# Optimization experiments

Hardware: AMD Instinct MI355X
Metric: run time of the kernel (lower is better)

Reference implementation:

```python
import jax, jax.numpy as jnp
import numpy as np

B, N, G, K, C, H, L = 16, 8192, 128, 32, 384, 6, 12
HID = 4 * C
EPS = 1e-5

def _pairwise_sq(a, b):
    # squared euclidean distances (B, M, N); same argsort order as torch.cdist
    d = (jnp.sum(a * a, -1)[:, :, None] + jnp.sum(b * b, -1)[:, None, :]
         - 2.0 * jnp.einsum('bmd,bnd->bmn', a, b))
    return jnp.maximum(d, 0.0)

def _fps(xyz, npoint):
    # deterministic farthest point sampling (start index 0), per torch loop
    bsz, n = xyz.shape[0], xyz.shape[1]
    def step(carry, _):
        distance, farthest = carry
        centroid = jnp.take_along_axis(xyz, farthest[:, None, None], axis=1)  # (B,1,3)
        d = jnp.sum((xyz - centroid) ** 2, axis=-1)
        distance = jnp.minimum(distance, d)
        nxt = jnp.argmax(distance, axis=-1).astype(jnp.int32)
        return (distance, nxt), farthest
    init = (jnp.full((bsz, n), 1e10, jnp.float32), jnp.zeros((bsz,), jnp.int32))
    _, cents = jax.lax.scan(step, init, None, length=npoint)
    return cents.T  # (B, npoint)

def _nearest_order(center):
    # greedy nearest-neighbor path over patch centers starting at 0
    bsz, g = center.shape[0], center.shape[1]
    d2 = _pairwise_sq(center, center)
    diag = jnp.arange(g)
    d2 = d2.at[:, diag, diag].set(jnp.inf)
    bi = jnp.arange(bsz)
    visited0 = jnp.zeros((bsz, g), bool).at[:, 0].set(True)
    def step(carry, _):
        last, visited = carry
        d = jnp.where(visited, jnp.inf, d2[bi, last])
        nxt = jnp.argmin(d, axis=-1).astype(jnp.int32)
        return (nxt, visited.at[bi, nxt].set(True)), nxt
    _, rest = jax.lax.scan(step, (jnp.zeros((bsz,), jnp.int32), visited0), None, length=g - 1)
    return jnp.concatenate([jnp.zeros((bsz, 1), jnp.int32), rest.T], axis=1)

def _bn(x, g, b):
    # BatchNorm1d, training-mode batch statistics over (batch, length)
    m = x.mean(axis=(0, 1))
    v = x.var(axis=(0, 1))
    return (x - m) * jax.lax.rsqrt(v + EPS) * g + b

def _ln(x, g, b):
    m = x.mean(-1, keepdims=True)
    v = x.var(-1, keepdims=True)
    return (x - m) * jax.lax.rsqrt(v + EPS) * g + b

def _pos_sine(coords, d_model):
    # sine/cosine positional embedding per coordinate channel (DETR-style)
    d_per = d_model // coords.shape[-1]  # 128 per xyz channel
    inv = 1.0 / (10000.0 ** (2.0 * jnp.arange(d_per // 2, dtype=jnp.float32) / d_per))
    ang = coords[..., None] * inv  # (B,G,3,d_per//2)
    emb = jnp.stack([jnp.sin(ang), jnp.cos(ang)], axis=-1)
    return emb.reshape(coords.shape[0], coords.shape[1], d_model)

def _block(x, mask, ln1g, ln1b, qkvw, qkvb, ow, ob, ln2g, ln2b, m1w, m1b, m2w, m2b):
    bsz, s, c = x.shape
    dh = c // H
    y = _ln(x, ln1g, ln1b)
    qkv = y @ qkvw.T + qkvb
    q, k, v = [t.reshape(bsz, s, H, dh) for t in jnp.split(qkv, 3, axis=-1)]
    scores = jnp.einsum('bqhd,bkhd->bhqk', q, k) / np.sqrt(dh)
    scores = jnp.where(mask, scores, -1e9)  # causal attn_mask
    attn = jax.nn.softmax(scores, axis=-1)
    o = jnp.einsum('bhqk,bkhd->bqhd', attn, v).reshape(bsz, s, c)
    x = x + o @ ow.T + ob
    h = jax.nn.gelu(_ln(x, ln2g, ln2b) @ m1w.T + m1b, approximate=False)
    return x + h @ m2w.T + m2b

def _forward(xyz, ec1_w, ec1_b, bn1_g, bn1_b, ec2_w, ec2_b, sc1_w, sc1_b,
             bn2_g, bn2_b, sc2_w, sc2_b, sos, ln1_g, ln1_b, qkv_w, qkv_b,
             out_w, out_b, ln2_g, ln2_b, mlp1_w, mlp1_b, mlp2_w, mlp2_b,
             lnf_g, lnf_b):
    bsz = xyz.shape[0]
    # --- Group: FPS centers + kNN neighborhoods + nearest-path ordering ---
    cent_idx = _fps(xyz, G)                                         # (B,G)
    center = jnp.take_along_axis(xyz, cent_idx[..., None], axis=1)  # (B,G,3)
    d2 = _pairwise_sq(center, xyz)                                  # (B,G,N)
    _, knn = jax.lax.top_k(-d2, K)                                  # smallest distances
    neigh = jnp.take_along_axis(xyz, knn.reshape(bsz, G * K)[..., None], axis=1)
    neigh = neigh.reshape(bsz, G, K, 3) - center[:, :, None, :]
    order = _nearest_order(center)
    neigh = jnp.take_along_axis(neigh, order[:, :, None, None], axis=1)
    center = jnp.take_along_axis(center, order[:, :, None], axis=1)
    # --- EncoderSmall (1x1 convs == pointwise matmuls + max pooling) ---
    x = neigh.reshape(bsz * G, K, 3)
    f = jax.nn.relu(_bn(x @ ec1_w.T + ec1_b, bn1_g, bn1_b))
    f = f @ ec2_w.T + ec2_b                                         # (BG,K,256)
    gmax = f.max(axis=1, keepdims=True)
    f = jnp.concatenate([jnp.broadcast_to(gmax, f.shape), f], axis=-1)  # (BG,K,512)
    f = jax.nn.relu(_bn(f @ sc1_w.T + sc1_b, bn2_g, bn2_b))
    f = f @ sc2_w.T + sc2_b
    tokens = f.max(axis=1).reshape(bsz, G, C)
    # --- GPT extractor: sos-shifted tokens, pos added per layer, causal ---
    pos = _pos_sine(center, C)
    mask = jnp.tril(jnp.ones((G, G), bool))
    h = jnp.concatenate([jnp.broadcast_to(sos, (bsz, 1, C)), tokens[:, :-1]], axis=1)
    for i in range(L):
        h = _block(h + pos, mask, ln1_g[i], ln1_b[i], qkv_w[i], qkv_b[i],
                   out_w[i], out_b[i], ln2_g[i], ln2_b[i], mlp1_w[i], mlp1_b[i],
                   mlp2_w[i], mlp2_b[i])
    return _ln(h, lnf_g, lnf_b)

def setup_inputs():
    key = jax.random.key(0)
    ks = jax.random.split(key, 12)
    w = lambda k, shape: jax.random.normal(k, shape, jnp.float32) * 0.02
    return {
        'xyz': jax.random.normal(ks[0], (B, N, 3), jnp.float32),
        'ec1_w': w(ks[1], (128, 3)), 'ec1_b': jnp.zeros((128,)),
        'bn1_g': jnp.ones((128,)), 'bn1_b': jnp.zeros((128,)),
        'ec2_w': w(ks[2], (256, 128)), 'ec2_b': jnp.zeros((256,)),
        'sc1_w': w(ks[3], (512, 512)), 'sc1_b': jnp.zeros((512,)),
        'bn2_g': jnp.ones((512,)), 'bn2_b': jnp.zeros((512,)),
        'sc2_w': w(ks[4], (C, 512)), 'sc2_b': jnp.zeros((C,)),
        'sos': w(ks[5], (1, 1, C)),
        'ln1_g': jnp.ones((L, C)), 'ln1_b': jnp.zeros((L, C)),
        'qkv_w': w(ks[6], (L, 3 * C, C)), 'qkv_b': jnp.zeros((L, 3 * C)),
        'out_w': w(ks[7], (L, C, C)), 'out_b': jnp.zeros((L, C)),
        'ln2_g': jnp.ones((L, C)), 'ln2_b': jnp.zeros((L, C)),
        'mlp1_w': w(ks[8], (L, HID, C)), 'mlp1_b': jnp.zeros((L, HID)),
        'mlp2_w': w(ks[9], (L, C, HID)), 'mlp2_b': jnp.zeros((L, C)),
        'lnf_g': jnp.ones((C,)), 'lnf_b': jnp.zeros((C,)),
    }

def reference(xyz, ec1_w, ec1_b, bn1_g, bn1_b, ec2_w, ec2_b, sc1_w, sc1_b,
              bn2_g, bn2_b, sc2_w, sc2_b, sos, ln1_g, ln1_b, qkv_w, qkv_b,
              out_w, out_b, ln2_g, ln2_b, mlp1_w, mlp1_b, mlp2_w, mlp2_b,
              lnf_g, lnf_b):
    return _forward(xyz, ec1_w, ec1_b, bn1_g, bn1_b, ec2_w, ec2_b, sc1_w, sc1_b,
                    bn2_g, bn2_b, sc2_w, sc2_b, sos, ln1_g, ln1_b, qkv_w, qkv_b,
                    out_w, out_b, ln2_g, ln2_b, mlp1_w, mlp1_b, mlp2_w, mlp2_b,
                    lnf_g, lnf_b)
```

## Files before the change

### kernel.cpp

```cpp
#include <hip/hip_runtime.h>
#include <math.h>

#define DEVFN __device__ __forceinline__

constexpr int NB   = 16;
constexpr int NPTS = 8192;
constexpr int NG   = 128;
constexpr int NK   = 32;
constexpr int NC   = 384;
constexpr int NH   = 6;
constexpr int NL   = 12;
constexpr int NHID = 1536;
constexpr int NDH  = 64;
constexpr float LN_EPS = 1e-5f;

typedef __attribute__((ext_vector_type(8))) short short8v;
typedef __attribute__((ext_vector_type(4))) float f32x4;
typedef unsigned long long u64;

DEVFN float sq3(float x, float y, float z) {
  return __fadd_rn(__fadd_rn(__fmul_rn(x, x), __fmul_rn(y, y)), __fmul_rn(z, z));
}
DEVFN float dot3(float ax, float ay, float az, float bx, float by, float bz) {
  return __fadd_rn(__fadd_rn(__fmul_rn(ax, bx), __fmul_rn(ay, by)), __fmul_rn(az, bz));
}
DEVFN unsigned short f2bf(float f) {
  unsigned u = __float_as_uint(f);
  return (unsigned short)((u + 0x7fffu + ((u >> 16) & 1u)) >> 16);
}
DEVFN float bf2f(unsigned short u) { return __uint_as_float(((unsigned)u) << 16); }

__global__ __launch_bounds__(512) void fps_kernel(const float* __restrict__ xyz,
                                                  int* __restrict__ cent) {
  extern __shared__ float dsm[];
  float* lx = dsm; float* ly = dsm + NPTS; float* lz = dsm + 2 * NPTS;
  __shared__ u64 swk[2][8];
  const int b = blockIdx.x, t = threadIdx.x;
  const float* X = xyz + (size_t)b * NPTS * 3;
  float px[16], py[16], pz[16], dd[16];
#pragma unroll
  for (int k = 0; k < 16; ++k) {
    const int i = t + k * 512;
    px[k] = X[i * 3 + 0]; py[k] = X[i * 3 + 1]; pz[k] = X[i * 3 + 2];
    lx[i] = px[k]; ly[i] = py[k]; lz[i] = pz[k];
    dd[k] = 1e10f;
  }
  __syncthreads();
  int far = 0;
  float fx = lx[0], fy = ly[0], fz = lz[0];
  for (int s = 0; s < NG; ++s) {
    if (t == 0) cent[b * NG + s] = far;
    float bv = -1.0f; int bi = 0;
#pragma unroll
    for (int k = 0; k < 16; ++k) {
      const float dx = __fsub_rn(px[k], fx);
      const float dy = __fsub_rn(py[k], fy);
      const float dz = __fsub_rn(pz[k], fz);
      const float d  = sq3(dx, dy, dz);
      const float nd = fminf(dd[k], d);
      dd[k] = nd;
      if (nd > bv) { bv = nd; bi = t + k * 512; }
    }
    u64 key = (((u64)__float_as_uint(bv)) << 32) | (unsigned)(8191 - bi);
#pragma unroll
    for (int m = 1; m < 64; m <<= 1) {
      const u64 o = __shfl_xor(key, m, 64);
      key = (o > key) ? o : key;
    }
    if ((t & 63) == 0) swk[s & 1][t >> 6] = key;
    __syncthreads();
    u64 fk = swk[s & 1][0];
#pragma unroll
    for (int w = 1; w < 8; ++w) fk = (swk[s & 1][w] > fk) ? swk[s & 1][w] : fk;
    far = 8191 - (int)(fk & 0xffffffffu);
    fx = lx[far]; fy = ly[far]; fz = lz[far];
  }
}

__global__ __launch_bounds__(256) void knn_kernel(const float* __restrict__ xyz,
                                                  const int* __restrict__ cent,
                                                  float* __restrict__ center,
                                                  int* __restrict__ knn) {
  __shared__ u64 swk[2][4];
  __shared__ float sc[3];
  const int bg = blockIdx.x, t = threadIdx.x;
  const int b = bg >> 7;
  const float* X = xyz + (size_t)b * NPTS * 3;
  if (t == 0) {
    const int ci = cent[bg];
    sc[0] = X[ci * 3 + 0]; sc[1] = X[ci * 3 + 1]; sc[2] = X[ci * 3 + 2];
    center[bg * 3 + 0] = sc[0]; center[bg * 3 + 1] = sc[1]; center[bg * 3 + 2] = sc[2];
  }
  __syncthreads();
  const float cx = sc[0], cy = sc[1], cz = sc[2];
  const float ra = sq3(cx, cy, cz);
  float d[32];
#pragma unroll
  for (int k = 0; k < 32; ++k) {
    const int i = t + k * 256;
    const float x = X[i * 3 + 0], y = X[i * 3 + 1], z = X[i * 3 + 2];
    const float rb = sq3(x, y, z);
    const float dt = dot3(cx, cy, cz, x, y, z);
    d[k] = fmaxf(__fsub_rn(__fadd_rn(ra, rb), __fmul_rn(2.0f, dt)), 0.0f);
  }
  float lv = 3.0e38f; int li = 0;
#pragma unroll
  for (int k = 0; k < 32; ++k) { if (d[k] < lv) { lv = d[k]; li = k; } }
  for (int k = 0; k < NK; ++k) {
    u64 key = (((u64)__float_as_uint(lv)) << 32) | (unsigned)(t + li * 256);
#pragma unroll
    for (int m = 1; m < 64; m <<= 1) {
      const u64 o = __shfl_xor(key, m, 64);
      key = (o < key) ? o : key;
    }
    if ((t & 63) == 0) swk[k & 1][t >> 6] = key;
    __syncthreads();
    u64 fk = swk[k & 1][0];
#pragma unroll
    for (int w = 1; w < 4; ++w) fk = (swk[k & 1][w] < fk) ? swk[k & 1][w] : fk;
    const int fi = (int)(fk & 0xffffffffu);
    if (t == 0) knn[(size_t)bg * NK + k] = fi;
    if ((fi & 255) == t) {
      const int kk = fi >> 8;
#pragma unroll
      for (int j = 0; j < 32; ++j) if (j == kk) d[j] = 3.0e38f;
      lv = 3.0e38f; li = 0;
#pragma unroll
      for (int j = 0; j < 32; ++j) { if (d[j] < lv) { lv = d[j]; li = j; } }
    }
  }
}

__global__ __launch_bounds__(128) void order_kernel(const float* __restrict__ center,
                                                    int* __restrict__ order) {
  __shared__ float cx[NG], cy[NG], cz[NG];
  __shared__ u64 swk[2][2];
  const int b = blockIdx.x, t = threadIdx.x;
  cx[t] = center[((size_t)b * NG + t) * 3 + 0];
  cy[t] = center[((size_t)b * NG + t) * 3 + 1];
  cz[t] = center[((size_t)b * NG + t) * 3 + 2];
  bool vis = (t == 0);
  if (t == 0) order[b * NG] = 0;
  __syncthreads();
  int last = 0;
  for (int s = 1; s < NG; ++s) {
    float dv;
    const float lx = cx[last], ly = cy[last], lz = cz[last];
    if (vis) {
      dv = 3.0e38f;
    } else {
      const float ra = sq3(lx, ly, lz), rb = sq3(cx[t], cy[t], cz[t]);
      const float dd = __fsub_rn(__fadd_rn(ra, rb),
                                 __fmul_rn(2.0f, dot3(lx, ly, lz, cx[t], cy[t], cz[t])));
      dv = fmaxf(dd, 0.0f);
    }
    u64 key = (((u64)__float_as_uint(dv)) << 32) | (unsigned)t;
#pragma unroll
    for (int m = 1; m < 64; m <<= 1) {
      const u64 o = __shfl_xor(key, m, 64);
      key = (o < key) ? o : key;
    }
    if ((t & 63) == 0) swk[s & 1][t >> 6] = key;
    __syncthreads();
    const u64 fk = (swk[s & 1][1] < swk[s & 1][0]) ? swk[s & 1][1] : swk[s & 1][0];
    last = (int)(fk & 0xffffffffu);
    if (t == last) vis = true;
    if (t == 0) order[b * NG + s] = last;
  }
}

__global__ void gather_neigh(const float* __restrict__ xyz, const int* __restrict__ knn,
                             const int* __restrict__ order, const float* __restrict__ center,
                             float* __restrict__ neigh, float* __restrict__ cord) {
  const int bg = blockIdx.x, t = threadIdx.x;
  const int b = bg >> 7;
  const int src = order[bg];
  const int sbg = (b << 7) + src;
  const float c0 = center[sbg * 3 + 0], c1 = center[sbg * 3 + 1], c2 = center[sbg * 3 + 2];
  if (t < 3) cord[bg * 3 + t] = center[sbg * 3 + t];
  const int idx = knn[(size_t)sbg * NK + t];
  const float* P = xyz + ((size_t)b * NPTS + idx) * 3;
  float* o = neigh + ((size_t)bg * NK + t) * 3;
  o[0] = __fsub_rn(P[0], c0);
  o[1] = __fsub_rn(P[1], c1);
  o[2] = __fsub_rn(P[2], c2);
}

__global__ __launch_bounds__(128) void bn1_stats(const float* __restrict__ neigh,
                                                 const float* __restrict__ w,
                                                 const float* __restrict__ bias,
                                                 float* __restrict__ psum,
                                                 float* __restrict__ psq) {
  const int c = threadIdx.x, blk = blockIdx.x;
  const float wx = w[c * 3 + 0], wy = w[c * 3 + 1], wz = w[c * 3 + 2], bb = bias[c];
  float s = 0.f, s2 = 0.f;
  const float* nr = neigh + (size_t)blk * 256 * 3;
  for (int r = 0; r < 256; ++r) {
    float y = fmaf(nr[r * 3 + 2], wz, fmaf(nr[r * 3 + 1], wy, fmaf(nr[r * 3 + 0], wx, bb)));
    s += y; s2 = fmaf(y, y, s2);
  }
  psum[c * 256 + blk] = s;
  psq[c * 256 + blk]  = s2;
}

__global__ __launch_bounds__(256) void bn_reduce(const float* __restrict__ psum,
                                                 const float* __restrict__ psq,
                                                 const float* __restrict__ g,
                                                 const float* __restrict__ b,
                                                 float* __restrict__ A, float* __restrict__ B0,
                                                 int P) {
  __shared__ double rs[256], rq[256];
  const int c = blockIdx.x, t = threadIdx.x;
  double s = 0.0, q = 0.0;
  for (int i = t; i < P; i += 256) {
    s += (double)psum[(size_t)c * P + i];
    q += (double)psq[(size_t)c * P + i];
  }
  rs[t] = s; rq[t] = q;
  __syncthreads();
  for (int o = 128; o > 0; o >>= 1) {
    if (t < o) { rs[t] += rs[t + o]; rq[t] += rq[t + o]; }
    __syncthreads();
  }
  if (t == 0) {
    const double M = 65536.0;
    double m = rs[0] / M;
    double v = rq[0] / M - m * m;
    if (v < 0) v = 0;
    float a = g[c] * rsqrtf((float)v + LN_EPS);
    A[c] = a;
    B0[c] = b[c] - (float)m * a;
  }
}

__global__ __launch_bounds__(256) void enc_f1(const float* __restrict__ neigh,
                                              const float* __restrict__ ec1w, const float* __restrict__ ec1b,
                                              const float* __restrict__ A1, const float* __restrict__ B01,
                                              unsigned short* __restrict__ f1bf) {
  __shared__ float ns[96];
  const int bg = blockIdx.x, t = threadIdx.x;
  if (t < 96) ns[t] = neigh[(size_t)bg * 96 + t];
  __syncthreads();
  for (int e = t; e < 32 * 128; e += 256) {
    const int r = e >> 7, c = e & 127;
    float y = fmaf(ns[r * 3 + 2], ec1w[c * 3 + 2],
             fmaf(ns[r * 3 + 1], ec1w[c * 3 + 1],
             fmaf(ns[r * 3 + 0], ec1w[c * 3 + 0], ec1b[c])));
    y = fmaxf(fmaf(y, A1[c], B01[c]), 0.f);
    f1bf[(size_t)bg * 4096 + e] = f2bf(y);
  }
}

template <int K, int NTILE, int EPI>
__global__ __launch_bounds__(256) void enc_gemm(const unsigned short* __restrict__ A,
                                                const unsigned short* __restrict__ W,
                                                const float* __restrict__ bias,
                                                const float* __restrict__ sgbuf,
                                                const float* __restrict__ A2,
                                                const float* __restrict__ B02,
                                                unsigned short* __restrict__ C,
                                                unsigned short* __restrict__ gmaxOut,
                                                float* __restrict__ psum,
                                                float* __restrict__ psq,
                                                const float* __restrict__ sc2b,
                                                float* __restrict__ tokens) {
  constexpr int LDA = K + 8;
  __shared__ unsigned short At[64 * LDA];
  const int blk = blockIdx.x, t = threadIdx.x;
  const int m0 = blk * 64;
  for (int idx = t; idx < 64 * (K / 8); idx += 256) {
    const int row = idx / (K / 8), off = idx % (K / 8);
    short8v v = *(const short8v*)(A + (size_t)(m0 + row) * K + off * 8);
    if (EPI == 2) {
      float a2v[8], b0v[8];
      *(float4*)(a2v)     = *(const float4*)(A2 + off * 8);
      *(float4*)(a2v + 4) = *(const float4*)(A2 + off * 8 + 4);
      *(float4*)(b0v)     = *(const float4*)(B02 + off * 8);
      *(float4*)(b0v + 4) = *(const float4*)(B02 + off * 8 + 4);
#pragma unroll
      for (int j = 0; j < 8; ++j)
        v[j] = (short)f2bf(fmaxf(fmaf(bf2f((unsigned short)v[j]), a2v[j], b0v[j]), 0.f));
    }
    *(short8v*)(At + row * LDA + off * 8) = v;
  }
  __syncthreads();
  const int lane = t & 63, wid = t >> 6;
  const int wr = wid >> 1, wc = wid & 1;
  const int lr = lane & 15, kg = lane >> 4;
  const int group = 2 * blk + wr;
  const unsigned short* a0 = At + (wr * 32 + lr) * LDA + kg * 8;
  const unsigned short* a1 = a0 + 16 * LDA;
  for (int nt = 0; nt < NTILE / 64; ++nt) {
    const int n0 = nt * 64 + wc * 32;
    const unsigned short* b0 = W + (size_t)(n0 + lr) * K + kg * 8;
    const unsigned short* b1 = b0 + (size_t)16 * K;
    f32x4 acc00 = {0.f, 0.f, 0.f, 0.f}, acc01 = acc00, acc10 = acc00, acc11 = acc00;
#pragma unroll
    for (int k0 = 0; k0 < K; k0 += 32) {
      const short8v av0 = *(const short8v*)(a0 + k0);
      const short8v av1 = *(const short8v*)(a1 + k0);
      const short8v bv0 = *(const short8v*)(b0 + k0);
      const short8v bv1 = *(const short8v*)(b1 + k0);
      acc00 = __builtin_amdgcn_mfma_f32_16x16x32_bf16(av0, bv0, acc00, 0, 0, 0);
      acc01 = __builtin_amdgcn_mfma_f32_16x16x32_bf16(av0, bv1, acc01, 0, 0, 0);
      acc10 = __builtin_amdgcn_mfma_f32_16x16x32_bf16(av1, bv0, acc10, 0, 0, 0);
      acc11 = __builtin_amdgcn_mfma_f32_16x16x32_bf16(av1, bv1, acc11, 0, 0, 0);
    }
#pragma unroll
    for (int j = 0; j < 2; ++j) {
      const int n = n0 + j * 16 + lr;
      float red0 = (EPI == 1) ? 0.f : -3.0e38f;
      float red1 = 0.f;
      float base = 0.f;
      if (EPI == 0) base = bias[n];
      if (EPI == 1) base = bias[n] + sgbuf[(size_t)group * NTILE + n];
#pragma unroll
      for (int i = 0; i < 2; ++i) {
        const f32x4 a = (i == 0) ? (j == 0 ? acc00 : acc01) : (j == 0 ? acc10 : acc11);
#pragma unroll
        for (int r = 0; r < 4; ++r) {
          const int m = m0 + wr * 32 + i * 16 + kg * 4 + r;
          const float v = a[r] + base;
          if (EPI == 0) {
            C[(size_t)m * NTILE + n] = f2bf(v);
            red0 = fmaxf(red0, v);
          } else if (EPI == 1) {
            const unsigned short us = f2bf(v);
            C[(size_t)m * NTILE + n] = us;
            const float vv = bf2f(us);
            red0 += vv; red1 = fmaf(vv, vv, red1);
          } else {
            red0 = fmaxf(red0, v);
          }
        }
      }
      if (EPI == 1) {
        red0 += __shfl_xor(red0, 16, 64); red0 += __shfl_xor(red0, 32, 64);
        red1 += __shfl_xor(red1, 16, 64); red1 += __shfl_xor(red1, 32, 64);
        if (kg == 0) {
          psum[(size_t)n * 2048 + blk * 2 + wr] = red0;
          psq[(size_t)n * 2048 + blk * 2 + wr]  = red1;
        }
      } else {
        red0 = fmaxf(red0, __shfl_xor(red0, 16, 64));
        red0 = fmaxf(red0, __shfl_xor(red0, 32, 64));
        if (kg == 0) {
          if (EPI == 0) gmaxOut[(size_t)group * NTILE + n] = f2bf(red0);
          else          tokens[(size_t)group * NTILE + n] = red0 + sc2b[n];
        }
      }
    }
  }
}

__global__ void pos_hinit(const float* __restrict__ cord, const float* __restrict__ tokens,
                          const float* __restrict__ sos,
                          float* __restrict__ pos, float* __restrict__ h) {
  const int tok = blockIdx.x, t = threadIdx.x;
  const int c = t >> 7;
  const int rem = t & 127;
  const int i = rem >> 1;
  const int isc = rem & 1;
  const float coord = cord[tok * 3 + c];
  const float ex = 2.0f * (float)i / 128.0f;
  const float inv = 1.0f / powf(10000.0f, ex);
  const float ang = coord * inv;
  pos[(size_t)tok * NC + t] = isc ? cosf(ang) : sinf(ang);
  const int b = tok >> 7, g = tok & 127;
  h[(size_t)tok * NC + t] = (g == 0) ? sos[t] : tokens[((size_t)b * NG + (g - 1)) * NC + t];
}

__global__ void cvt_all(const float* __restrict__ qkvw, const float* __restrict__ outw,
                        const float* __restrict__ m1w, const float* __restrict__ m2w,
                        const float* __restrict__ ec2w, const float* __restrict__ sc1w,
                        const float* __restrict__ sc2w,
                        unsigned short* __restrict__ wqkv, unsigned short* __restrict__ wout,
                        unsigned short* __restrict__ wm1, unsigned short* __restrict__ wm2,
                        unsigned short* __restrict__ ec2, unsigned short* __restrict__ w3a,
                        unsigned short* __restrict__ w3b, unsigned short* __restrict__ sc2) {
  constexpr int S0 = NL * 3 * NC * NC;
  constexpr int O0 = S0;
  constexpr int O1 = O0 + NL * NC * NC;
  constexpr int O2 = O1 + NL * NHID * NC;
  constexpr int O3 = O2 + NL * NC * NHID;
  constexpr int O4 = O3 + 256 * 128;
  constexpr int O5 = O4 + 512 * 512;
  constexpr int TOT = O5 + 384 * 512;
  for (int i = blockIdx.x * blockDim.x + threadIdx.x; i < TOT; i += gridDim.x * blockDim.x) {
    if (i < O0)      wqkv[i] = f2bf(qkvw[i]);
    else if (i < O1) wout[i - O0] = f2bf(outw[i - O0]);
    else if (i < O2) wm1[i - O1] = f2bf(m1w[i - O1]);
    else if (i < O3) wm2[i - O2] = f2bf(m2w[i - O2]);
    else if (i < O4) ec2[i - O3] = f2bf(ec2w[i - O3]);
    else if (i < O5) {
      const int ii = i - O4, c = ii >> 9, k = ii & 511;
      const unsigned short v = f2bf(sc1w[ii]);
      if (k < 256) w3a[c * 256 + k] = v;
      else         w3b[c * 256 + (k - 256)] = v;
    } else sc2[i - O5] = f2bf(sc2w[i - O5]);
  }
}

template <bool BF16OUT>
__global__ __launch_bounds__(128) void ln_kernel(const float* __restrict__ in,
                                                 const float* __restrict__ add,
                                                 const float* __restrict__ g,
                                                 const float* __restrict__ b,
                                                 void* __restrict__ y,
                                                 float* __restrict__ xout) {
  __shared__ float sm[4];
  const int row = blockIdx.x, t = threadIdx.x, w = t >> 6;
  const float* ip = in + (size_t)row * NC;
  float v0 = ip[t], v1 = ip[t + 128], v2 = ip[t + 256];
  if (add) {
    const float* ap = add + (size_t)row * NC;
    v0 += ap[t]; v1 += ap[t + 128]; v2 += ap[t + 256];
  }
  float s = v0 + v1 + v2;
#pragma unroll
  for (int m = 1; m < 64; m <<= 1) s += __shfl_xor(s, m, 64);
  if ((t & 63) == 0) sm[w] = s;
  __syncthreads();
  const float mean = (sm[0] + sm[1]) / (float)NC;
  const float d0 = v0 - mean, d1 = v1 - mean, d2 = v2 - mean;
  float sq = d0 * d0 + d1 * d1 + d2 * d2;
#pragma unroll
  for (int m = 1; m < 64; m <<= 1) sq += __shfl_xor(sq, m, 64);
  if ((t & 63) == 0) sm[2 + w] = sq;
  __syncthreads();
  const float rs = rsqrtf((sm[2] + sm[3]) / (float)NC + LN_EPS);
  const float y0 = d0 * rs * g[t] + b[t];
  const float y1 = d1 * rs * g[t + 128] + b[t + 128];
  const float y2 = d2 * rs * g[t + 256] + b[t + 256];
  if (BF16OUT) {
    unsigned short* yp = (unsigned short*)y + (size_t)row * NC;
    yp[t] = f2bf(y0); yp[t + 128] = f2bf(y1); yp[t + 256] = f2bf(y2);
  } else {
    float* yp = (float*)y + (size_t)row * NC;
    yp[t] = y0; yp[t + 128] = y1; yp[t + 256] = y2;
  }
  if (xout) {
    float* xp = xout + (size_t)row * NC;
    xp[t] = v0; xp[t + 128] = v1; xp[t + 256] = v2;
  }
}

template <int ACT, int RESMODE, bool OUT_BF, int K>
__global__ __launch_bounds__(256) void gemm_mfma(const unsigned short* __restrict__ A,
                                                 const unsigned short* __restrict__ W,
                                                 const float* __restrict__ bias,
                                                 const float* __restrict__ R,
                                                 void* __restrict__ Cv,
                                                 int N) {
  const int t = threadIdx.x;
  const int lane = t & 63, wid = t >> 6;
  const int wr = wid >> 1, wc = wid & 1;
  const int m0 = blockIdx.y * 64 + wr * 32;
  const int n0 = blockIdx.x * 64 + wc * 32;
  const int lr = lane & 15, kg = lane >> 4;
  const unsigned short* a0p = A + (size_t)(m0 + lr) * K + kg * 8;
  const unsigned short* a1p = a0p + (size_t)16 * K;
  const unsigned short* b0p = W + (size_t)(n0 + lr) * K + kg * 8;
  const unsigned short* b1p = b0p + (size_t)16 * K;
  f32x4 acc00 = {0.f, 0.f, 0.f, 0.f}, acc01 = acc00, acc10 = acc00, acc11 = acc00;
#pragma unroll 2
  for (int k0 = 0; k0 < K; k0 += 32) {
    const short8v av0 = *(const short8v*)(a0p + k0);
    const short8v av1 = *(const short8v*)(a1p + k0);
    const short8v bv0 = *(const short8v*)(b0p + k0);
    const short8v bv1 = *(const short8v*)(b1p + k0);
    acc00 = __builtin_amdgcn_mfma_f32_16x16x32_bf16(av0, bv0, acc00, 0, 0, 0);
    acc01 = __builtin_amdgcn_mfma_f32_16x16x32_bf16(av0, bv1, acc01, 0, 0, 0);
    acc10 = __builtin_amdgcn_mfma_f32_16x16x32_bf16(av1, bv0, acc10, 0, 0, 0);
    acc11 = __builtin_amdgcn_mfma_f32_16x16x32_bf16(av1, bv1, acc11, 0, 0, 0);
  }
#pragma unroll
  for (int i = 0; i < 2; ++i) {
#pragma unroll
    for (int j = 0; j < 2; ++j) {
      const f32x4 a = (i == 0) ? (j == 0 ? acc00 : acc01) : (j == 0 ? acc10 : acc11);
      const int n = n0 + j * 16 + lr;
      const float bn = bias ? bias[n] : 0.f;
#pragma unroll
      for (int r = 0; r < 4; ++r) {
        const int m = m0 + i * 16 + kg * 4 + r;
        float v = a[r] + bn;
        if (ACT == 1) v = 0.5f * v * (1.0f + erff(v * 0.70710678118654752f));
        if (RESMODE == 1) v += R[(size_t)m * N + n];
        if (OUT_BF) ((unsigned short*)Cv)[(size_t)m * N + n] = f2bf(v);
        else        ((float*)Cv)[(size_t)m * N + n] = v;
      }
    }
  }
}

__global__ __launch_bounds__(256) void attn_fused(const unsigned short* __restrict__ qkv,
                                                  unsigned short* __restrict__ obuf) {
  __shared__ __align__(16) unsigned short qs[64 * 72];
  __shared__ __align__(16) unsigned short ks[128 * 72];
  __shared__ __align__(16) unsigned short vt[64 * 136];
  __shared__ __align__(16) unsigned short ps[64 * 136];
  const int blk = blockIdx.x, t = threadIdx.x;
  const int qt = blk & 1;
  const int h = (blk >> 1) % NH;
  const int b = blk / (2 * NH);
  const size_t qbase = ((size_t)(b * NG + qt * 64)) * (3 * NC) + h * NDH;
  const size_t kbase = ((size_t)(b * NG)) * (3 * NC) + NC + h * NDH;
  const size_t vbase = kbase + NC;
#pragma unroll
  for (int it = 0; it < 2; ++it) {
    const int idx = t + it * 256;
    const int r = idx >> 3, c0 = (idx & 7) * 8;
    *(short8v*)(qs + r * 72 + c0) = *(const short8v*)(qkv + qbase + (size_t)r * (3 * NC) + c0);
  }
#pragma unroll
  for (int it = 0; it < 4; ++it) {
    const int idx = t + it * 256;
    const int r = idx >> 3, c0 = (idx & 7) * 8;
    *(short8v*)(ks + r * 72 + c0) = *(const short8v*)(qkv + kbase + (size_t)r * (3 * NC) + c0);
  }
#pragma unroll
  for (int it = 0; it < 4; ++it) {
    const int idx = t + it * 256;
    const int r = idx >> 3, c0 = (idx & 7) * 8;
    const short8v v = *(const short8v*)(qkv + vbase + (size_t)r * (3 * NC) + c0);
#pragma unroll
    for (int j = 0; j < 8; ++j) vt[(c0 + j) * 136 + r] = (unsigned short)v[j];
  }
  __syncthreads();
  const int lane = t & 63, w = t >> 6;
  const int lr = lane & 15, kg = lane >> 4;
  f32x4 sc[8] = {};
  {
    const short8v av0 = *(const short8v*)(qs + (w * 16 + lr) * 72 + kg * 8);
    const short8v av1 = *(const short8v*)(qs + (w * 16 + lr) * 72 + 32 + kg * 8);
#pragma unroll
    for (int j = 0; j < 8; ++j) {
      const short8v bv0 = *(const short8v*)(ks + (j * 16 + lr) * 72 + kg * 8);
      const short8v bv1 = *(const short8v*)(ks + (j * 16 + lr) * 72 + 32 + kg * 8);
      sc[j] = __builtin_amdgcn_mfma_f32_16x16x32_bf16(av0, bv0, sc[j], 0, 0, 0);
      sc[j] = __builtin_amdgcn_mfma_f32_16x16x32_bf16(av1, bv1, sc[j], 0, 0, 0);
    }
  }
#pragma unroll
  for (int r = 0; r < 4; ++r) {
    const int rowg = qt * 64 + w * 16 + kg * 4 + r;
    float pj[8];
    float mx = -3.0e38f;
#pragma unroll
    for (int j = 0; j < 8; ++j) {
      const int col = j * 16 + lr;
      const float s = (col <= rowg) ? sc[j][r] * 0.125f : -1e9f;
      pj[j] = s;
      mx = fmaxf(mx, s);
    }
#pragma unroll
    for (int m = 1; m < 16; m <<= 1) mx = fmaxf(mx, __shfl_xor(mx, m, 64));
    float sum = 0.f;
#pragma unroll
    for (int j = 0; j < 8; ++j) { pj[j] = expf(pj[j] - mx); sum += pj[j]; }
#pragma unroll
    for (int m = 1; m < 16; m <<= 1) sum += __shfl_xor(sum, m, 64);
#pragma unroll
    for (int j = 0; j < 8; ++j)
      ps[(w * 16 + kg * 4 + r) * 136 + j * 16 + lr] = f2bf(pj[j] / sum);
  }
  __syncthreads();
  f32x4 oc[4] = {};
#pragma unroll
  for (int k = 0; k < 4; ++k) {
    const short8v av = *(const short8v*)(ps + (w * 16 + lr) * 136 + k * 32 + kg * 8);
#pragma unroll
    for (int dj = 0; dj < 4; ++dj) {
      const short8v bv = *(const short8v*)(vt + (dj * 16 + lr) * 136 + k * 32 + kg * 8);
      oc[dj] = __builtin_amdgcn_mfma_f32_16x16x32_bf16(av, bv, oc[dj], 0, 0, 0);
    }
  }
#pragma unroll
  for (int dj = 0; dj < 4; ++dj) {
#pragma unroll
    for (int r = 0; r < 4; ++r) {
      const int m = qt * 64 + w * 16 + kg * 4 + r;
      obuf[((size_t)(b * NG + m)) * NC + h * NDH + dj * 16 + lr] = f2bf(oc[dj][r]);
    }
  }
}

extern "C" void kernel_launch(void* const* d_in, const int* in_sizes, int n_in,
                              void* d_out, int out_size, void* d_ws, size_t ws_size,
                              hipStream_t stream) {
  (void)in_sizes; (void)n_in; (void)out_size; (void)ws_size;
  const float* xyz  = (const float*)d_in[0];
  const float* ec1w = (const float*)d_in[1];
  const float* ec1b = (const float*)d_in[2];
  const float* bn1g = (const float*)d_in[3];
  const float* bn1b = (const float*)d_in[4];
  const float* ec2w = (const float*)d_in[5];
  const float* ec2b = (const float*)d_in[6];
  const float* sc1w = (const float*)d_in[7];
  const float* sc1b = (const float*)d_in[8];
  const float* bn2g = (const float*)d_in[9];
  const float* bn2b = (const float*)d_in[10];
  const float* sc2w = (const float*)d_in[11];
  const float* sc2b = (const float*)d_in[12];
  const float* sos  = (const float*)d_in[13];
  const float* ln1g = (const float*)d_in[14];
  const float* ln1b = (const float*)d_in[15];
  const float* qkvw = (const float*)d_in[16];
  const float* qkvb = (const float*)d_in[17];
  const float* outw = (const float*)d_in[18];
  const float* outb = (const float*)d_in[19];
  const float* ln2g = (const float*)d_in[20];
  const float* ln2b = (const float*)d_in[21];
  const float* m1w  = (const float*)d_in[22];
  const float* m1b  = (const float*)d_in[23];
  const float* m2w  = (const float*)d_in[24];
  const float* m2b  = (const float*)d_in[25];
  const float* lnfg = (const float*)d_in[26];
  const float* lnfb = (const float*)d_in[27];
  float* out = (float*)d_out;

  char* p = (char*)d_ws;
  auto carve = [&](size_t bytes) -> void* {
    void* q = (void*)p;
    p += (bytes + 255) & ~(size_t)255;
    return q;
  };
  int*   cent   = (int*)carve((size_t)NB * NG * 4);
  float* center = (float*)carve((size_t)NB * NG * 3 * 4);
  int*   knn    = (int*)carve((size_t)NB * NG * NK * 4);
  int*   order  = (int*)carve((size_t)NB * NG * 4);
  float* neigh  = (float*)carve((size_t)NB * NG * NK * 3 * 4);
  float* cord   = (float*)carve((size_t)NB * NG * 3 * 4);
  float* psum1  = (float*)carve((size_t)128 * 256 * 4);
  float* psq1   = (float*)carve((size_t)128 * 256 * 4);
  float* A1     = (float*)carve(128 * 4);
  float* B01    = (float*)carve(128 * 4);
  float* psum2  = (float*)carve((size_t)512 * 2048 * 4);
  float* psq2   = (float*)carve((size_t)512 * 2048 * 4);
  float* A2     = (float*)carve(512 * 4);
  float* B02    = (float*)carve(512 * 4);
  float* tokens = (float*)carve((size_t)NB * NG * NC * 4);
  float* posb   = (float*)carve((size_t)NB * NG * NC * 4);
  float* hbuf   = (float*)carve((size_t)NB * NG * NC * 4);
  float* xbuf   = (float*)carve((size_t)NB * NG * NC * 4);
  unsigned short* ybf    = (unsigned short*)carve((size_t)NB * NG * NC * 2);
  unsigned short* qkv_bf = (unsigned short*)carve((size_t)NB * NG * 3 * NC * 2);
  unsigned short* obf    = (unsigned short*)carve((size_t)NB * NG * NC * 2);
  unsigned short* mh_bf  = (unsigned short*)carve((size_t)NB * NG * NHID * 2);
  unsigned short* wqkv_bf = (unsigned short*)carve((size_t)NL * 3 * NC * NC * 2);
  unsigned short* wout_bf = (unsigned short*)carve((size_t)NL * NC * NC * 2);
  unsigned short* wm1_bf  = (unsigned short*)carve((size_t)NL * NHID * NC * 2);
  unsigned short* wm2_bf  = (unsigned short*)carve((size_t)NL * NC * NHID * 2);
  unsigned short* ec2w_bf = (unsigned short*)carve((size_t)256 * 128 * 2);
  unsigned short* w3a_bf  = (unsigned short*)carve((size_t)512 * 256 * 2);
  unsigned short* w3b_bf  = (unsigned short*)carve((size_t)512 * 256 * 2);
  unsigned short* sc2w_bf = (unsigned short*)carve((size_t)384 * 512 * 2);
  unsigned short* f1bf   = (unsigned short*)carve((size_t)65536 * 128 * 2);
  unsigned short* f2bf_a = (unsigned short*)carve((size_t)65536 * 256 * 2);
  unsigned short* gmaxbf = (unsigned short*)carve((size_t)2048 * 256 * 2);
  float*          sgbuf  = (float*)carve((size_t)2048 * 512 * 4);
  unsigned short* s3bf   = (unsigned short*)carve((size_t)65536 * 512 * 2);

  const int NTOK = NB * NG;

  cvt_all<<<2048, 256, 0, stream>>>(qkvw, outw, m1w, m2w, ec2w, sc1w, sc2w,
                                    wqkv_bf, wout_bf, wm1_bf, wm2_bf,
                                    ec2w_bf, w3a_bf, w3b_bf, sc2w_bf);

  fps_kernel<<<NB, 512, 3 * NPTS * 4, stream>>>(xyz, cent);
  knn_kernel<<<NTOK, 256, 0, stream>>>(xyz, cent, center, knn);
  order_kernel<<<NB, 128, 0, stream>>>(center, order);
  gather_neigh<<<NTOK, 32, 0, stream>>>(xyz, knn, order, center, neigh, cord);

  bn1_stats<<<256, 128, 0, stream>>>(neigh, ec1w, ec1b, psum1, psq1);
  bn_reduce<<<128, 256, 0, stream>>>(psum1, psq1, bn1g, bn1b, A1, B01, 256);
  enc_f1<<<NTOK, 256, 0, stream>>>(neigh, ec1w, ec1b, A1, B01, f1bf);
  enc_gemm<128, 256, 0><<<1024, 256, 0, stream>>>(
      f1bf, ec2w_bf, ec2b, nullptr, nullptr, nullptr,
      f2bf_a, gmaxbf, nullptr, nullptr, nullptr, nullptr);
  gemm_mfma<0, 0, false, 256><<<dim3(8, 32), 256, 0, stream>>>(
      gmaxbf, w3a_bf, nullptr, nullptr, sgbuf, 512);
  enc_gemm<256, 512, 1><<<1024, 256, 0, stream>>>(
      f2bf_a, w3b_bf, sc1b, sgbuf, nullptr, nullptr,
      s3bf, nullptr, psum2, psq2, nullptr, nullptr);
  bn_reduce<<<512, 256, 0, stream>>>(psum2, psq2, bn2g, bn2b, A2, B02, 2048);
  enc_gemm<512, 384, 2><<<1024, 256, 0, stream>>>(
      s3bf, sc2w_bf, nullptr, nullptr, A2, B02,
      nullptr, nullptr, nullptr, nullptr, sc2b, tokens);

  pos_hinit<<<NTOK, NC, 0, stream>>>(cord, tokens, sos, posb, hbuf);

  for (int l = 0; l < NL; ++l) {
    ln_kernel<true><<<NTOK, 128, 0, stream>>>(hbuf, posb, ln1g + l * NC, ln1b + l * NC, ybf, xbuf);
    gemm_mfma<0, 0, true, 384><<<dim3(18, 32), 256, 0, stream>>>(
        ybf, wqkv_bf + (size_t)l * 3 * NC * NC, qkvb + (size_t)l * 3 * NC, nullptr, qkv_bf,
        3 * NC);
    attn_fused<<<NB * NH * 2, 256, 0, stream>>>(qkv_bf, obf);
    gemm_mfma<0, 1, false, 384><<<dim3(6, 32), 256, 0, stream>>>(
        obf, wout_bf + (size_t)l * NC * NC, outb + (size_t)l * NC, xbuf, hbuf, NC);
    ln_kernel<true><<<NTOK, 128, 0, stream>>>(hbuf, nullptr, ln2g + l * NC, ln2b + l * NC, ybf, nullptr);
    gemm_mfma<1, 0, true, 384><<<dim3(24, 32), 256, 0, stream>>>(
        ybf, wm1_bf + (size_t)l * NHID * NC, m1b + (size_t)l * NHID, nullptr, mh_bf, NHID);
    gemm_mfma<0, 1, false, 1536><<<dim3(6, 32), 256, 0, stream>>>(
        mh_bf, wm2_bf + (size_t)l * NC * NHID, m2b + (size_t)l * NC, hbuf, hbuf, NC);
  }
  ln_kernel<false><<<NTOK, 128, 0, stream>>>(hbuf, nullptr, lnfg, lnfb, out, nullptr);
}
```

Baseline: 1.629 ms.

## Drop xbuf residual copy, widen enc_gemm N-tile, deepen gemm unroll

The LN1 kernel no longer writes a float copy of h+pos. The out-projection GEMM instead adds hbuf and posb directly in a new residual mode, which removes one full-activation write and read per layer. Separately, the encoder GEMM now computes four 16-wide N sub-tiles per wave instead of two, reusing the A fragments across more MFMAs at the cost of more accumulator registers. The transformer GEMM K-loop unroll goes from 2 to 4. The first change relies on the out-projection reading hbuf and posb before writing hbuf in place; each element is read and written by the same thread, so this stays correct.

```diff
diff --git a/kernel.cpp b/kernel.cpp
--- a/kernel.cpp
+++ b/kernel.cpp
@@ -290,24 +290,22 @@
   const int group = 2 * blk + wr;
   const unsigned short* a0 = At + (wr * 32 + lr) * LDA + kg * 8;
   const unsigned short* a1 = a0 + 16 * LDA;
-  for (int nt = 0; nt < NTILE / 64; ++nt) {
-    const int n0 = nt * 64 + wc * 32;
-    const unsigned short* b0 = W + (size_t)(n0 + lr) * K + kg * 8;
-    const unsigned short* b1 = b0 + (size_t)16 * K;
-    f32x4 acc00 = {0.f, 0.f, 0.f, 0.f}, acc01 = acc00, acc10 = acc00, acc11 = acc00;
+  for (int nt = 0; nt < NTILE / 128; ++nt) {
+    const int n0 = nt * 128 + wc * 64;
+    f32x4 acc[2][4] = {};
 #pragma unroll
     for (int k0 = 0; k0 < K; k0 += 32) {
       const short8v av0 = *(const short8v*)(a0 + k0);
       const short8v av1 = *(const short8v*)(a1 + k0);
-      const short8v bv0 = *(const short8v*)(b0 + k0);
-      const short8v bv1 = *(const short8v*)(b1 + k0);
-      acc00 = __builtin_amdgcn_mfma_f32_16x16x32_bf16(av0, bv0, acc00, 0, 0, 0);
-      acc01 = __builtin_amdgcn_mfma_f32_16x16x32_bf16(av0, bv1, acc01, 0, 0, 0);
-      acc10 = __builtin_amdgcn_mfma_f32_16x16x32_bf16(av1, bv0, acc10, 0, 0, 0);
-      acc11 = __builtin_amdgcn_mfma_f32_16x16x32_bf16(av1, bv1, acc11, 0, 0, 0);
-    }
-#pragma unroll
-    for (int j = 0; j < 2; ++j) {
+#pragma unroll
+      for (int j = 0; j < 4; ++j) {
+        const short8v bv = *(const short8v*)(W + (size_t)(n0 + j * 16 + lr) * K + kg * 8 + k0);
+        acc[0][j] = __builtin_amdgcn_mfma_f32_16x16x32_bf16(av0, bv, acc[0][j], 0, 0, 0);
+        acc[1][j] = __builtin_amdgcn_mfma_f32_16x16x32_bf16(av1, bv, acc[1][j], 0, 0, 0);
+      }
+    }
+#pragma unroll
+    for (int j = 0; j < 4; ++j) {
       const int n = n0 + j * 16 + lr;
       float red0 = (EPI == 1) ? 0.f : -3.0e38f;
       float red1 = 0.f;
@@ -316,11 +314,10 @@
       if (EPI == 1) base = bias[n] + sgbuf[(size_t)group * NTILE + n];
 #pragma unroll
       for (int i = 0; i < 2; ++i) {
-        const f32x4 a = (i == 0) ? (j == 0 ? acc00 : acc01) : (j == 0 ? acc10 : acc11);
 #pragma unroll
         for (int r = 0; r < 4; ++r) {
           const int m = m0 + wr * 32 + i * 16 + kg * 4 + r;
-          const float v = a[r] + base;
+          const float v = acc[i][j][r] + base;
           if (EPI == 0) {
             C[(size_t)m * NTILE + n] = f2bf(v);
             red0 = fmaxf(red0, v);
@@ -406,8 +403,7 @@
                                                  const float* __restrict__ add,
                                                  const float* __restrict__ g,
                                                  const float* __restrict__ b,
-                                                 void* __restrict__ y,
-                                                 float* __restrict__ xout) {
+                                                 void* __restrict__ y) {
   __shared__ float sm[4];
   const int row = blockIdx.x, t = threadIdx.x, w = t >> 6;
   const float* ip = in + (size_t)row * NC;
@@ -439,10 +435,6 @@
     float* yp = (float*)y + (size_t)row * NC;
     yp[t] = y0; yp[t + 128] = y1; yp[t + 256] = y2;
   }
-  if (xout) {
-    float* xp = xout + (size_t)row * NC;
-    xp[t] = v0; xp[t + 128] = v1; xp[t + 256] = v2;
-  }
 }
 
 template <int ACT, int RESMODE, bool OUT_BF, int K>
@@ -450,6 +442,7 @@
                                                  const unsigned short* __restrict__ W,
                                                  const float* __restrict__ bias,
                                                  const float* __restrict__ R,
+                                                 const float* __restrict__ R2,
                                                  void* __restrict__ Cv,
                                                  int N) {
   const int t = threadIdx.x;
@@ -463,7 +456,7 @@
   const unsigned short* b0p = W + (size_t)(n0 + lr) * K + kg * 8;
   const unsigned short* b1p = b0p + (size_t)16 * K;
   f32x4 acc00 = {0.f, 0.f, 0.f, 0.f}, acc01 = acc00, acc10 = acc00, acc11 = acc00;
-#pragma unroll 2
+#pragma unroll 4
   for (int k0 = 0; k0 < K; k0 += 32) {
     const short8v av0 = *(const short8v*)(a0p + k0);
     const short8v av1 = *(const short8v*)(a1p + k0);
@@ -487,6 +480,7 @@
         float v = a[r] + bn;
         if (ACT == 1) v = 0.5f * v * (1.0f + erff(v * 0.70710678118654752f));
         if (RESMODE == 1) v += R[(size_t)m * N + n];
+        if (RESMODE == 3) v += R[(size_t)m * N + n] + R2[(size_t)m * N + n];
         if (OUT_BF) ((unsigned short*)Cv)[(size_t)m * N + n] = f2bf(v);
         else        ((float*)Cv)[(size_t)m * N + n] = v;
       }
@@ -643,7 +637,6 @@
   float* tokens = (float*)carve((size_t)NB * NG * NC * 4);
   float* posb   = (float*)carve((size_t)NB * NG * NC * 4);
   float* hbuf   = (float*)carve((size_t)NB * NG * NC * 4);
-  float* xbuf   = (float*)carve((size_t)NB * NG * NC * 4);
   unsigned short* ybf    = (unsigned short*)carve((size_t)NB * NG * NC * 2);
   unsigned short* qkv_bf = (unsigned short*)carve((size_t)NB * NG * 3 * NC * 2);
   unsigned short* obf    = (unsigned short*)carve((size_t)NB * NG * NC * 2);
@@ -680,7 +673,7 @@
       f1bf, ec2w_bf, ec2b, nullptr, nullptr, nullptr,
       f2bf_a, gmaxbf, nullptr, nullptr, nullptr, nullptr);
   gemm_mfma<0, 0, false, 256><<<dim3(8, 32), 256, 0, stream>>>(
-      gmaxbf, w3a_bf, nullptr, nullptr, sgbuf, 512);
+      gmaxbf, w3a_bf, nullptr, nullptr, nullptr, sgbuf, 512);
   enc_gemm<256, 512, 1><<<1024, 256, 0, stream>>>(
       f2bf_a, w3b_bf, sc1b, sgbuf, nullptr, nullptr,
       s3bf, nullptr, psum2, psq2, nullptr, nullptr);
@@ -692,18 +685,19 @@
   pos_hinit<<<NTOK, NC, 0, stream>>>(cord, tokens, sos, posb, hbuf);
 
   for (int l = 0; l < NL; ++l) {
-    ln_kernel<true><<<NTOK, 128, 0, stream>>>(hbuf, posb, ln1g + l * NC, ln1b + l * NC, ybf, xbuf);
+    ln_kernel<true><<<NTOK, 128, 0, stream>>>(hbuf, posb, ln1g + l * NC, ln1b + l * NC, ybf);
     gemm_mfma<0, 0, true, 384><<<dim3(18, 32), 256, 0, stream>>>(
-        ybf, wqkv_bf + (size_t)l * 3 * NC * NC, qkvb + (size_t)l * 3 * NC, nullptr, qkv_bf,
-        3 * NC);
+        ybf, wqkv_bf + (size_t)l * 3 * NC * NC, qkvb + (size_t)l * 3 * NC, nullptr, nullptr,
+        qkv_bf, 3 * NC);
     attn_fused<<<NB * NH * 2, 256, 0, stream>>>(qkv_bf, obf);
-    gemm_mfma<0, 1, false, 384><<<dim3(6, 32), 256, 0, stream>>>(
-        obf, wout_bf + (size_t)l * NC * NC, outb + (size_t)l * NC, xbuf, hbuf, NC);
-    ln_kernel<true><<<NTOK, 128, 0, stream>>>(hbuf, nullptr, ln2g + l * NC, ln2b + l * NC, ybf, nullptr);
+    gemm_mfma<0, 3, false, 384><<<dim3(6, 32), 256, 0, stream>>>(
+        obf, wout_bf + (size_t)l * NC * NC, outb + (size_t)l * NC, hbuf, posb, hbuf, NC);
+    ln_kernel<true><<<NTOK, 128, 0, stream>>>(hbuf, nullptr, ln2g + l * NC, ln2b + l * NC, ybf);
     gemm_mfma<1, 0, true, 384><<<dim3(24, 32), 256, 0, stream>>>(
-        ybf, wm1_bf + (size_t)l * NHID * NC, m1b + (size_t)l * NHID, nullptr, mh_bf, NHID);
+        ybf, wm1_bf + (size_t)l * NHID * NC, m1b + (size_t)l * NHID, nullptr, nullptr,
+        mh_bf, NHID);
     gemm_mfma<0, 1, false, 1536><<<dim3(6, 32), 256, 0, stream>>>(
-        mh_bf, wm2_bf + (size_t)l * NC * NHID, m2b + (size_t)l * NC, hbuf, hbuf, NC);
-  }
-  ln_kernel<false><<<NTOK, 128, 0, stream>>>(hbuf, nullptr, lnfg, lnfb, out, nullptr);
-}
+        mh_bf, wm2_bf + (size_t)l * NC * NHID, m2b + (size_t)l * NC, hbuf, nullptr, hbuf, NC);
+  }
+  ln_kernel<false><<<NTOK, 128, 0, stream>>>(hbuf, nullptr, lnfg, lnfb, out);
+}
```

Measured after the change: 1.692 ms, median of 2. 3.9% more time.
